# Optimization experiments

Hardware: AMD Instinct MI355X
Metric: run time of the kernel (lower is better)

Reference implementation:

```python
import jax, jax.numpy as jnp
import numpy as np

EMBED = 1024
HEADS = 16
HEAD_DIM = EMBED // HEADS


def setup_inputs() -> dict:
    key = jax.random.key(0)
    ks = jax.random.split(key, 11)
    s = 1.0 / np.sqrt(EMBED)
    B, L = 4, 2048
    return {
        "query": jax.random.normal(ks[0], (B, L, EMBED), jnp.float32),
        "key":   jax.random.normal(ks[1], (B, L, EMBED), jnp.float32),
        "value": jax.random.normal(ks[2], (B, L, EMBED), jnp.float32),
        "Wq": jax.random.normal(ks[3], (EMBED, EMBED), jnp.float32) * s,
        "bq": jnp.zeros((EMBED,), jnp.float32),
        "Wk": jax.random.normal(ks[4], (EMBED, EMBED), jnp.float32) * s,
        "bk": jnp.zeros((EMBED,), jnp.float32),
        "Wv": jax.random.normal(ks[5], (EMBED, EMBED), jnp.float32) * s,
        "bv": jnp.zeros((EMBED,), jnp.float32),
        "Wo": jax.random.normal(ks[6], (EMBED, EMBED), jnp.float32) * s,
        "bo": jnp.zeros((EMBED,), jnp.float32),
    }


def reference(query, key, value, Wq, bq, Wk, bk, Wv, bv, Wo, bo):
    N, Lq, E = query.shape
    Lk = key.shape[1]
    # linear projections (torch nn.Linear: x @ W.T + b)
    q = (query @ Wq.T + bq).reshape(N, Lq, HEADS, HEAD_DIM)
    k = (key   @ Wk.T + bk).reshape(N, Lk, HEADS, HEAD_DIM)
    v = (value @ Wv.T + bv).reshape(N, Lk, HEADS, HEAD_DIM)
    # scaled dot-product attention; note: original scales by sqrt(embed_size)
    scale = 1.0 / jnp.sqrt(jnp.float32(E))
    energy = jnp.einsum('nqhd,nkhd->nhqk', q, k) * scale  # [N,H,Lq,Lk]
    score = jax.nn.softmax(energy, axis=-1)
    out = jnp.einsum('nhqk,nkhd->nqhd', score, v).reshape(N, Lq, E)
    return out @ Wo.T + bo
```

## Files before the change

kernel.cpp:

```cpp
#include <hip/hip_runtime.h>
#include <stdint.h>

#define EMBED 1024
#define HEADS 16
#define HDIM 64
#define BATCH 4
#define SEQ 2048
#define ROWS (BATCH*SEQ)
#define QROWS 128

typedef __attribute__((ext_vector_type(8))) __bf16 bf16x8;
typedef __attribute__((ext_vector_type(4))) float f32x4;

#define LDS_U32(p) ((__attribute__((address_space(3))) unsigned int*)(p))
#define GLB_U32(p) ((const __attribute__((address_space(1))) unsigned int*)(p))

__device__ inline unsigned short f2bf(float f) {
    union { float f; unsigned int u; } v; v.f = f;
    unsigned int u = v.u;
    return (unsigned short)((u + 0x7FFFu + ((u >> 16) & 1u)) >> 16);
}

__global__ __launch_bounds__(256) void cvt3(const float* __restrict__ s0, const float* __restrict__ s1,
                                            const float* __restrict__ s2,
                                            unsigned short* __restrict__ d0, unsigned short* __restrict__ d1,
                                            unsigned short* __restrict__ d2) {
    const float* src = (blockIdx.y == 0) ? s0 : (blockIdx.y == 1) ? s1 : s2;
    unsigned short* dst = (blockIdx.y == 0) ? d0 : (blockIdx.y == 1) ? d1 : d2;
    int i = (blockIdx.x * 256 + threadIdx.x) * 4;
    float4 v = *(const float4*)(src + i);
    uint2 p;
    p.x = (unsigned)f2bf(v.x) | ((unsigned)f2bf(v.y) << 16);
    p.y = (unsigned)f2bf(v.z) | ((unsigned)f2bf(v.w) << 16);
    *(uint2*)(dst + i) = p;
}
__global__ __launch_bounds__(256) void cvt4(const float* __restrict__ s0, const float* __restrict__ s1,
                                            const float* __restrict__ s2, const float* __restrict__ s3,
                                            unsigned short* __restrict__ dst, int stride) {
    const float* src = (blockIdx.y == 0) ? s0 : (blockIdx.y == 1) ? s1 : (blockIdx.y == 2) ? s2 : s3;
    unsigned short* d = dst + (size_t)blockIdx.y * stride;
    int i = (blockIdx.x * 256 + threadIdx.x) * 4;
    float4 v = *(const float4*)(src + i);
    uint2 p;
    p.x = (unsigned)f2bf(v.x) | ((unsigned)f2bf(v.y) << 16);
    p.y = (unsigned)f2bf(v.z) | ((unsigned)f2bf(v.w) << 16);
    *(uint2*)(d + i) = p;
}

template <bool OUT_BF16, bool QKV>
__global__ __launch_bounds__(256) void gemm_bt(const unsigned short* __restrict__ A0,
                                               const unsigned short* __restrict__ B0,
                                               const float* __restrict__ bias0,
                                               const float* __restrict__ bias1,
                                               const float* __restrict__ bias2,
                                               void* __restrict__ C0,
                                               float scale0,
                                               int M, int N, int K) {
    __shared__ unsigned short As[128 * 64];
    __shared__ unsigned short Bs[128 * 64];

    const int tid  = threadIdx.x;
    const int lane = tid & 63;
    const int wave = tid >> 6;
    const int l15  = lane & 15;
    const int quad = lane >> 4;
    const int wm   = wave & 1;
    const int wn   = wave >> 1;

    const unsigned nx = gridDim.x, ny = gridDim.y;
    const unsigned nwg = nx * ny * gridDim.z;
    const unsigned lin = (blockIdx.z * ny + blockIdx.y) * nx + blockIdx.x;
    const unsigned swz = (lin & 7) * (nwg >> 3) + (lin >> 3);
    const unsigned bx = swz % nx;
    const unsigned rem = swz / nx;
    const unsigned by = rem % ny;
    const unsigned bz = rem / ny;

    const int tileM = by * 128;
    const int tileN = bx * 128;

    const unsigned short* A = A0;
    const unsigned short* B = B0;
    const float* bias = bias0;
    void* C = C0;
    float scale = QKV ? scale0 : 1.0f;
    if (QKV) {
        int z = bz;
        A = A0 + (size_t)z * M * K;
        B = B0 + (size_t)z * N * K;
        bias = (z == 0) ? bias0 : (z == 1) ? bias1 : bias2;
        C = (void*)((unsigned short*)C0 + (size_t)z * M * N);
        if (z != 0) scale = 1.0f;
    }

    f32x4 acc[4][4] = {};

    for (int k0 = 0; k0 < K; k0 += 64) {
        __syncthreads();
#pragma unroll
        for (int s = 0; s < 4; ++s) {
            int j = tid + s * 256;
            int r = j >> 3;
            int c8 = (j & 7) ^ (r & 7);
            __builtin_amdgcn_global_load_lds(GLB_U32(A + (size_t)(tileM + r) * K + k0 + c8 * 8),
                                             LDS_U32(As + j * 8), 16, 0, 0);
            __builtin_amdgcn_global_load_lds(GLB_U32(B + (size_t)(tileN + r) * K + k0 + c8 * 8),
                                             LDS_U32(Bs + j * 8), 16, 0, 0);
        }
        __syncthreads();

#pragma unroll
        for (int kc = 0; kc < 2; ++kc) {
            bf16x8 a[4], b[4];
#pragma unroll
            for (int i = 0; i < 4; ++i) {
                int ra = wm * 64 + i * 16 + l15;
                a[i] = *(const bf16x8*)(As + ra * 64 + (((kc * 4 + quad) ^ (ra & 7)) * 8));
                int rb = wn * 64 + i * 16 + l15;
                b[i] = *(const bf16x8*)(Bs + rb * 64 + (((kc * 4 + quad) ^ (rb & 7)) * 8));
            }
#pragma unroll
            for (int i = 0; i < 4; ++i)
#pragma unroll
                for (int jn = 0; jn < 4; ++jn)
                    acc[i][jn] = __builtin_amdgcn_mfma_f32_16x16x32_bf16(a[i], b[jn], acc[i][jn], 0, 0, 0);
        }
    }

#pragma unroll
    for (int i = 0; i < 4; ++i) {
        int row0 = tileM + wm * 64 + i * 16 + (quad << 2);
#pragma unroll
        for (int jn = 0; jn < 4; ++jn) {
            int col = tileN + wn * 64 + jn * 16 + l15;
            float bv = bias[col];
#pragma unroll
            for (int r = 0; r < 4; ++r) {
                float v = (acc[i][jn][r] + bv) * scale;
                if (OUT_BF16)
                    ((unsigned short*)C)[(size_t)(row0 + r) * N + col] = f2bf(v);
                else
                    ((float*)C)[(size_t)(row0 + r) * N + col] = v;
            }
        }
    }
}

__global__ __launch_bounds__(256) void transpose_v(const unsigned short* __restrict__ src,
                                                   unsigned short* __restrict__ dst) {
    __shared__ unsigned short T[64 * 65];
    const int tid = threadIdx.x;
    const int st = blockIdx.x;
    const int h  = blockIdx.y;
    const int b  = blockIdx.z;

#pragma unroll
    for (int s = 0; s < 2; ++s) {
        int j = tid + s * 256;
        int r = j >> 3;
        int c = (j & 7) * 8;
        unsigned short tmp[8];
        *(uint4*)tmp = *(const uint4*)(src + ((size_t)b * SEQ + st * 64 + r) * EMBED + h * HDIM + c);
#pragma unroll
        for (int i = 0; i < 8; ++i)
            T[r * 65 + c + i] = tmp[i];
    }
    __syncthreads();
#pragma unroll
    for (int s = 0; s < 2; ++s) {
        int j = tid + s * 256;
        int d  = j >> 3;
        int c8 = (j & 7) * 8;
        unsigned short tmp[8];
#pragma unroll
        for (int i = 0; i < 8; ++i)
            tmp[i] = T[(c8 + i) * 65 + d];
        *(uint4*)(dst + ((size_t)(b * HEADS + h) * HDIM + d) * SEQ + st * 64 + c8) = *(uint4*)tmp;
    }
}

__global__ __launch_bounds__(256, 4) void attn(const unsigned short* __restrict__ Q,
                                               const unsigned short* __restrict__ Kp,
                                               const unsigned short* __restrict__ Vt,
                                               unsigned short* __restrict__ O) {
    __shared__ unsigned short KVs[2][2][64 * 64];

    const int tid  = threadIdx.x;
    const int lane = tid & 63;
    const int wave = tid >> 6;
    const int l15  = lane & 15;
    const int quad = lane >> 4;

    const int lin = ((blockIdx.z * HEADS + blockIdx.y) << 4) | blockIdx.x;
    const int swz = ((lin & 7) << 7) | (lin >> 3);
    const int qt = swz & 15;
    const int h  = (swz >> 4) & 15;
    const int b  = swz >> 8;

    const size_t rowbase = (size_t)b * SEQ;
    const int colbase = h * HDIM;
    const size_t vtbase = (size_t)(b * HEADS + h) * HDIM;

#pragma unroll
    for (int s = 0; s < 2; ++s) {
        int j = tid + s * 256;
        int r = j >> 3;
        int sr = (r & 35) | ((r & 12) << 1) | ((r & 16) >> 2);
        int c8 = (j & 7) ^ (r & 7);
        __builtin_amdgcn_global_load_lds(GLB_U32(Kp + (rowbase + sr) * EMBED + colbase + c8 * 8),
                                         LDS_U32(KVs[0][0] + j * 8), 16, 0, 0);
        __builtin_amdgcn_global_load_lds(GLB_U32(Vt + (vtbase + r) * SEQ + c8 * 8),
                                         LDS_U32(KVs[0][1] + j * 8), 16, 0, 0);
    }

    bf16x8 aq[2][2];
#pragma unroll
    for (int mf = 0; mf < 2; ++mf) {
        const unsigned short* qp =
            Q + (rowbase + qt * QROWS + wave * 32 + mf * 16 + l15) * EMBED + colbase;
#pragma unroll
        for (int ks = 0; ks < 2; ++ks)
            aq[mf][ks] = *(const bf16x8*)(qp + ks * 32 + quad * 8);
    }

    const f32x4 fz = {0.0f, 0.0f, 0.0f, 0.0f};
    bf16x8 vone;
#pragma unroll
    for (int i = 0; i < 8; ++i) vone[i] = (__bf16)1.0f;

    f32x4 oacc[2][4] = {};
    f32x4 sumacc[2] = {};

    for (int t = 0; t < 32; ++t) {
        __syncthreads();
        if (t + 1 < 32) {
            int nb = (t + 1) & 1;
#pragma unroll
            for (int s = 0; s < 2; ++s) {
                int j = tid + s * 256;
                int r = j >> 3;
                int sr = (r & 35) | ((r & 12) << 1) | ((r & 16) >> 2);
                int c8 = (j & 7) ^ (r & 7);
                __builtin_amdgcn_global_load_lds(GLB_U32(Kp + (rowbase + (t + 1) * 64 + sr) * EMBED + colbase + c8 * 8),
                                                 LDS_U32(KVs[nb][0] + j * 8), 16, 0, 0);
                __builtin_amdgcn_global_load_lds(GLB_U32(Vt + (vtbase + r) * SEQ + (t + 1) * 64 + c8 * 8),
                                                 LDS_U32(KVs[nb][1] + j * 8), 16, 0, 0);
            }
        }
        const unsigned short* Ks = KVs[t & 1][0];
        const unsigned short* Vs = KVs[t & 1][1];

        f32x4 sacc[2][4];
        __builtin_amdgcn_s_setprio(1);
#pragma unroll
        for (int nf = 0; nf < 4; ++nf) {
            int krow = nf * 16 + l15;
            int ch = quad ^ (krow & 7);
            bf16x8 bk = *(const bf16x8*)(Ks + krow * 64 + ch * 8);
            sacc[0][nf] = __builtin_amdgcn_mfma_f32_16x16x32_bf16(bk, aq[0][0], fz, 0, 0, 0);
            sacc[1][nf] = __builtin_amdgcn_mfma_f32_16x16x32_bf16(bk, aq[1][0], fz, 0, 0, 0);
        }
#pragma unroll
        for (int nf = 0; nf < 4; ++nf) {
            int krow = nf * 16 + l15;
            int ch = (4 + quad) ^ (krow & 7);
            bf16x8 bk = *(const bf16x8*)(Ks + krow * 64 + ch * 8);
            sacc[0][nf] = __builtin_amdgcn_mfma_f32_16x16x32_bf16(bk, aq[0][1], sacc[0][nf], 0, 0, 0);
            sacc[1][nf] = __builtin_amdgcn_mfma_f32_16x16x32_bf16(bk, aq[1][1], sacc[1][nf], 0, 0, 0);
        }
        __builtin_amdgcn_s_setprio(0);

        bf16x8 apv[2][2];
#pragma unroll
        for (int mf = 0; mf < 2; ++mf)
#pragma unroll
            for (int nf = 0; nf < 4; ++nf) {
                int ks2 = nf >> 1;
                int jb = (nf & 1) * 4;
                apv[mf][ks2][jb + 0] = (__bf16)__builtin_amdgcn_exp2f(sacc[mf][nf][0]);
                apv[mf][ks2][jb + 1] = (__bf16)__builtin_amdgcn_exp2f(sacc[mf][nf][1]);
                apv[mf][ks2][jb + 2] = (__bf16)__builtin_amdgcn_exp2f(sacc[mf][nf][2]);
                apv[mf][ks2][jb + 3] = (__bf16)__builtin_amdgcn_exp2f(sacc[mf][nf][3]);
            }

        __builtin_amdgcn_s_setprio(1);
#pragma unroll
        for (int ks = 0; ks < 2; ++ks) {
            sumacc[0] = __builtin_amdgcn_mfma_f32_16x16x32_bf16(apv[0][ks], vone, sumacc[0], 0, 0, 0);
            sumacc[1] = __builtin_amdgcn_mfma_f32_16x16x32_bf16(apv[1][ks], vone, sumacc[1], 0, 0, 0);
#pragma unroll
            for (int df = 0; df < 4; ++df) {
                int vrow = df * 16 + l15;
                int ch = (ks * 4 + quad) ^ (vrow & 7);
                bf16x8 bv = *(const bf16x8*)(Vs + vrow * 64 + ch * 8);
                oacc[0][df] = __builtin_amdgcn_mfma_f32_16x16x32_bf16(apv[0][ks], bv, oacc[0][df], 0, 0, 0);
                oacc[1][df] = __builtin_amdgcn_mfma_f32_16x16x32_bf16(apv[1][ks], bv, oacc[1][df], 0, 0, 0);
            }
        }
        __builtin_amdgcn_s_setprio(0);
    }

    float rinv[2][4];
#pragma unroll
    for (int mf = 0; mf < 2; ++mf)
#pragma unroll
        for (int r = 0; r < 4; ++r)
            rinv[mf][r] = 1.0f / sumacc[mf][r];

#pragma unroll
    for (int mf = 0; mf < 2; ++mf)
#pragma unroll
        for (int df = 0; df < 4; ++df) {
            int col = colbase + df * 16 + l15;
#pragma unroll
            for (int r = 0; r < 4; ++r) {
                int row = qt * QROWS + wave * 32 + mf * 16 + quad * 4 + r;
                O[(rowbase + row) * EMBED + col] = f2bf(oacc[mf][df][r] * rinv[mf][r]);
            }
        }
}

extern "C" void kernel_launch(void* const* d_in, const int* in_sizes, int n_in,
                              void* d_out, int out_size, void* d_ws, size_t ws_size,
                              hipStream_t stream) {
    const float* q_in = (const float*)d_in[0];
    const float* k_in = (const float*)d_in[1];
    const float* v_in = (const float*)d_in[2];
    const float* Wq = (const float*)d_in[3];
    const float* bq = (const float*)d_in[4];
    const float* Wk = (const float*)d_in[5];
    const float* bk = (const float*)d_in[6];
    const float* Wv = (const float*)d_in[7];
    const float* bv = (const float*)d_in[8];
    const float* Wo = (const float*)d_in[9];
    const float* bo = (const float*)d_in[10];
    float* out = (float*)d_out;

    const size_t XE = (size_t)ROWS * EMBED;
    const size_t WE = (size_t)EMBED * EMBED;

    unsigned short* ws = (unsigned short*)d_ws;
    unsigned short* xq = ws;
    unsigned short* xk = xq + XE;
    unsigned short* xv = xk + XE;
    unsigned short* wqkvo = xv + XE;
    unsigned short* wo = wqkvo + 3 * WE;
    unsigned short* Qp = wo + WE;
    unsigned short* Kp = Qp + XE;
    unsigned short* Vp = Kp + XE;
    unsigned short* Ap = Vp + XE;

    const float cexp = 0.045084436f;

    cvt3<<<dim3((unsigned)(XE / 1024), 3), 256, 0, stream>>>(q_in, k_in, v_in, xq, xk, xv);
    cvt4<<<dim3((unsigned)(WE / 1024), 4), 256, 0, stream>>>(Wq, Wk, Wv, Wo, wqkvo, (int)WE);

    gemm_bt<true, true><<<dim3(EMBED / 128, ROWS / 128, 3), 256, 0, stream>>>(
        xq, wqkvo, bq, bk, bv, Qp, cexp, ROWS, EMBED, EMBED);

    transpose_v<<<dim3(SEQ / 64, HEADS, BATCH), 256, 0, stream>>>(Vp, xv);

    attn<<<dim3(SEQ / QROWS, HEADS, BATCH), 256, 0, stream>>>(Qp, Kp, xv, Ap);

    gemm_bt<false, false><<<dim3(EMBED / 128, ROWS / 128), 256, 0, stream>>>(
        Ap, wo, bo, nullptr, nullptr, out, 1.0f, ROWS, EMBED, EMBED);
}
```

Before: 326.4 us.

## Fuse input bf16 conversion and V transpose into QKV projection GEMM

Removes the separate fp32-to-bf16 conversion kernel for the activations. The QKV GEMM now reads fp32 inputs directly and converts them while staging into shared memory. The V transpose kernel is also removed: the V slice of the GEMM writes its output already transposed into the per-head [d][seq] layout that attention consumes. This saves two launches and the round-trips through intermediate buffers. The cost is that the A-operand loads for the projection are now synchronous register loads of twice the bytes instead of async global-to-LDS copies, and the transposed V store is strided.

After: 340.7 us. 4.4% more time.

```diff
diff --git a/kernel.cpp b/kernel.cpp
--- a/kernel.cpp
+++ b/kernel.cpp
@@ -21,19 +21,6 @@
     return (unsigned short)((u + 0x7FFFu + ((u >> 16) & 1u)) >> 16);
 }
 
-__global__ __launch_bounds__(256) void cvt3(const float* __restrict__ s0, const float* __restrict__ s1,
-                                            const float* __restrict__ s2,
-                                            unsigned short* __restrict__ d0, unsigned short* __restrict__ d1,
-                                            unsigned short* __restrict__ d2) {
-    const float* src = (blockIdx.y == 0) ? s0 : (blockIdx.y == 1) ? s1 : s2;
-    unsigned short* dst = (blockIdx.y == 0) ? d0 : (blockIdx.y == 1) ? d1 : d2;
-    int i = (blockIdx.x * 256 + threadIdx.x) * 4;
-    float4 v = *(const float4*)(src + i);
-    uint2 p;
-    p.x = (unsigned)f2bf(v.x) | ((unsigned)f2bf(v.y) << 16);
-    p.y = (unsigned)f2bf(v.z) | ((unsigned)f2bf(v.w) << 16);
-    *(uint2*)(dst + i) = p;
-}
 __global__ __launch_bounds__(256) void cvt4(const float* __restrict__ s0, const float* __restrict__ s1,
                                             const float* __restrict__ s2, const float* __restrict__ s3,
                                             unsigned short* __restrict__ dst, int stride) {
@@ -48,12 +35,15 @@
 }
 
 template <bool OUT_BF16, bool QKV>
-__global__ __launch_bounds__(256) void gemm_bt(const unsigned short* __restrict__ A0,
+__global__ __launch_bounds__(256) void gemm_bt(const void* __restrict__ A0,
+                                               const void* __restrict__ A1,
+                                               const void* __restrict__ A2,
                                                const unsigned short* __restrict__ B0,
                                                const float* __restrict__ bias0,
                                                const float* __restrict__ bias1,
                                                const float* __restrict__ bias2,
                                                void* __restrict__ C0,
+                                               unsigned short* __restrict__ vtout,
                                                float scale0,
                                                int M, int N, int K) {
     __shared__ unsigned short As[128 * 64];
@@ -79,31 +69,59 @@
     const int tileM = by * 128;
     const int tileN = bx * 128;
 
-    const unsigned short* A = A0;
+    const float* Af = nullptr;
+    const unsigned short* Ab = nullptr;
     const unsigned short* B = B0;
     const float* bias = bias0;
     void* C = C0;
+    int z = 0;
     float scale = QKV ? scale0 : 1.0f;
     if (QKV) {
-        int z = bz;
-        A = A0 + (size_t)z * M * K;
+        z = bz;
+        Af = (z == 0) ? (const float*)A0 : (z == 1) ? (const float*)A1 : (const float*)A2;
         B = B0 + (size_t)z * N * K;
         bias = (z == 0) ? bias0 : (z == 1) ? bias1 : bias2;
         C = (void*)((unsigned short*)C0 + (size_t)z * M * N);
         if (z != 0) scale = 1.0f;
+    } else {
+        Ab = (const unsigned short*)A0;
     }
 
     f32x4 acc[4][4] = {};
 
     for (int k0 = 0; k0 < K; k0 += 64) {
         __syncthreads();
+        if (QKV) {
+#pragma unroll
+            for (int s = 0; s < 4; ++s) {
+                int j = tid + s * 256;
+                int r = j >> 3;
+                int c8 = (j & 7) ^ (r & 7);
+                const float* src = Af + (size_t)(tileM + r) * K + k0 + c8 * 8;
+                float4 lo = *(const float4*)(src);
+                float4 hi = *(const float4*)(src + 4);
+                bf16x8 v;
+                v[0] = (__bf16)lo.x; v[1] = (__bf16)lo.y;
+                v[2] = (__bf16)lo.z; v[3] = (__bf16)lo.w;
+                v[4] = (__bf16)hi.x; v[5] = (__bf16)hi.y;
+                v[6] = (__bf16)hi.z; v[7] = (__bf16)hi.w;
+                *(bf16x8*)(As + j * 8) = v;
+            }
+        } else {
+#pragma unroll
+            for (int s = 0; s < 4; ++s) {
+                int j = tid + s * 256;
+                int r = j >> 3;
+                int c8 = (j & 7) ^ (r & 7);
+                __builtin_amdgcn_global_load_lds(GLB_U32(Ab + (size_t)(tileM + r) * K + k0 + c8 * 8),
+                                                 LDS_U32(As + j * 8), 16, 0, 0);
+            }
+        }
 #pragma unroll
         for (int s = 0; s < 4; ++s) {
             int j = tid + s * 256;
             int r = j >> 3;
             int c8 = (j & 7) ^ (r & 7);
-            __builtin_amdgcn_global_load_lds(GLB_U32(A + (size_t)(tileM + r) * K + k0 + c8 * 8),
-                                             LDS_U32(As + j * 8), 16, 0, 0);
             __builtin_amdgcn_global_load_lds(GLB_U32(B + (size_t)(tileN + r) * K + k0 + c8 * 8),
                                              LDS_U32(Bs + j * 8), 16, 0, 0);
         }
@@ -127,55 +145,40 @@
         }
     }
 
-#pragma unroll
-    for (int i = 0; i < 4; ++i) {
-        int row0 = tileM + wm * 64 + i * 16 + (quad << 2);
-#pragma unroll
-        for (int jn = 0; jn < 4; ++jn) {
-            int col = tileN + wn * 64 + jn * 16 + l15;
-            float bv = bias[col];
-#pragma unroll
-            for (int r = 0; r < 4; ++r) {
-                float v = (acc[i][jn][r] + bv) * scale;
-                if (OUT_BF16)
-                    ((unsigned short*)C)[(size_t)(row0 + r) * N + col] = f2bf(v);
-                else
-                    ((float*)C)[(size_t)(row0 + r) * N + col] = v;
-            }
-        }
-    }
-}
-
-__global__ __launch_bounds__(256) void transpose_v(const unsigned short* __restrict__ src,
-                                                   unsigned short* __restrict__ dst) {
-    __shared__ unsigned short T[64 * 65];
-    const int tid = threadIdx.x;
-    const int st = blockIdx.x;
-    const int h  = blockIdx.y;
-    const int b  = blockIdx.z;
-
-#pragma unroll
-    for (int s = 0; s < 2; ++s) {
-        int j = tid + s * 256;
-        int r = j >> 3;
-        int c = (j & 7) * 8;
-        unsigned short tmp[8];
-        *(uint4*)tmp = *(const uint4*)(src + ((size_t)b * SEQ + st * 64 + r) * EMBED + h * HDIM + c);
-#pragma unroll
-        for (int i = 0; i < 8; ++i)
-            T[r * 65 + c + i] = tmp[i];
-    }
-    __syncthreads();
-#pragma unroll
-    for (int s = 0; s < 2; ++s) {
-        int j = tid + s * 256;
-        int d  = j >> 3;
-        int c8 = (j & 7) * 8;
-        unsigned short tmp[8];
-#pragma unroll
-        for (int i = 0; i < 8; ++i)
-            tmp[i] = T[(c8 + i) * 65 + d];
-        *(uint4*)(dst + ((size_t)(b * HEADS + h) * HDIM + d) * SEQ + st * 64 + c8) = *(uint4*)tmp;
+    if (QKV && z == 2) {
+#pragma unroll
+        for (int i = 0; i < 4; ++i) {
+            int row0 = tileM + wm * 64 + i * 16 + (quad << 2);
+            int bb   = row0 >> 11;
+            int seq0 = row0 & (SEQ - 1);
+#pragma unroll
+            for (int jn = 0; jn < 4; ++jn) {
+                int col = tileN + wn * 64 + jn * 16 + l15;
+                float bv = bias[col];
+                uint2 p;
+                p.x = (unsigned)f2bf(acc[i][jn][0] + bv) | ((unsigned)f2bf(acc[i][jn][1] + bv) << 16);
+                p.y = (unsigned)f2bf(acc[i][jn][2] + bv) | ((unsigned)f2bf(acc[i][jn][3] + bv) << 16);
+                *(uint2*)(vtout + ((size_t)(bb * HEADS) * HDIM + col) * SEQ + seq0) = p;
+            }
+        }
+    } else {
+#pragma unroll
+        for (int i = 0; i < 4; ++i) {
+            int row0 = tileM + wm * 64 + i * 16 + (quad << 2);
+#pragma unroll
+            for (int jn = 0; jn < 4; ++jn) {
+                int col = tileN + wn * 64 + jn * 16 + l15;
+                float bv = bias[col];
+#pragma unroll
+                for (int r = 0; r < 4; ++r) {
+                    float v = (acc[i][jn][r] + bv) * scale;
+                    if (OUT_BF16)
+                        ((unsigned short*)C)[(size_t)(row0 + r) * N + col] = f2bf(v);
+                    else
+                        ((float*)C)[(size_t)(row0 + r) * N + col] = v;
+                }
+            }
+        }
     }
 }
 
@@ -340,28 +343,22 @@
     const size_t WE = (size_t)EMBED * EMBED;
 
     unsigned short* ws = (unsigned short*)d_ws;
-    unsigned short* xq = ws;
-    unsigned short* xk = xq + XE;
-    unsigned short* xv = xk + XE;
-    unsigned short* wqkvo = xv + XE;
+    unsigned short* vt = ws;
+    unsigned short* wqkvo = vt + XE;
     unsigned short* wo = wqkvo + 3 * WE;
     unsigned short* Qp = wo + WE;
     unsigned short* Kp = Qp + XE;
-    unsigned short* Vp = Kp + XE;
-    unsigned short* Ap = Vp + XE;
+    unsigned short* Ap = Kp + XE;
 
     const float cexp = 0.045084436f;
 
-    cvt3<<<dim3((unsigned)(XE / 1024), 3), 256, 0, stream>>>(q_in, k_in, v_in, xq, xk, xv);
     cvt4<<<dim3((unsigned)(WE / 1024), 4), 256, 0, stream>>>(Wq, Wk, Wv, Wo, wqkvo, (int)WE);
 
     gemm_bt<true, true><<<dim3(EMBED / 128, ROWS / 128, 3), 256, 0, stream>>>(
-        xq, wqkvo, bq, bk, bv, Qp, cexp, ROWS, EMBED, EMBED);
-
-    transpose_v<<<dim3(SEQ / 64, HEADS, BATCH), 256, 0, stream>>>(Vp, xv);
-
-    attn<<<dim3(SEQ / QROWS, HEADS, BATCH), 256, 0, stream>>>(Qp, Kp, xv, Ap);
+        q_in, k_in, v_in, wqkvo, bq, bk, bv, Qp, vt, cexp, ROWS, EMBED, EMBED);
+
+    attn<<<dim3(SEQ / QROWS, HEADS, BATCH), 256, 0, stream>>>(Qp, Kp, vt, Ap);
 
     gemm_bt<false, false><<<dim3(EMBED / 128, ROWS / 128), 256, 0, stream>>>(
-        Ap, wo, bo, nullptr, nullptr, out, 1.0f, ROWS, EMBED, EMBED);
-}
+        Ap, nullptr, nullptr, wo, bo, nullptr, nullptr, out, nullptr, 1.0f, ROWS, EMBED, EMBED);
+}
```
